# Performance work log

Measured on AMD Instinct MI355X. Metric: run time of the kernel, lower is better.

The kernel has to match this reference:

```python
import jax, jax.numpy as jnp
import numpy as np

B, S, H = 4, 2048, 1024
E, I, K = 8, 2048, 2


def setup_inputs() -> dict:
    key = jax.random.key(0)
    ks = jax.random.split(key, 6)
    return {
        "hidden_states": jax.random.normal(ks[0], (B, S, H), dtype=jnp.float32),
        "Wg": jax.random.normal(ks[1], (H, E), dtype=jnp.float32) * 0.02,
        "W1": jax.random.normal(ks[2], (E, H, I), dtype=jnp.float32) * 0.02,
        "b1": jnp.zeros((E, I), dtype=jnp.float32),
        "W2": jax.random.normal(ks[3], (E, I, H), dtype=jnp.float32) * 0.02,
        "b2": jnp.zeros((E, H), dtype=jnp.float32),
    }


def reference(hidden_states, Wg, W1, b1, W2, b2):
    b, s, h = hidden_states.shape
    x = hidden_states.reshape(-1, h)                      # [T, H]
    gate_logits = x @ Wg                                  # [T, E]
    gate_probs = jax.nn.softmax(gate_logits, axis=-1)
    topk_probs, topk_idx = jax.lax.top_k(gate_probs, K)   # [T, K]
    topk_probs = topk_probs / jnp.sum(topk_probs, axis=-1, keepdims=True)
    # dense combine weights [T, E] (zero where expert not selected)
    T = x.shape[0]
    w = jnp.zeros((T, E), dtype=x.dtype)
    w = w.at[jnp.arange(T)[:, None], topk_idx].set(topk_probs)
    # run every expert on all tokens (dense grouped-GEMM form), exact erf GELU
    h1 = jax.nn.gelu(jnp.einsum('th,ehi->eti', x, W1) + b1[:, None, :], approximate=False)  # [E, T, I]
    y = jnp.einsum('eti,eih->eth', h1, W2) + b2[:, None, :]                                  # [E, T, H]
    out = jnp.einsum('te,eth->th', w, y)                                                     # [T, H]
    return out.reshape(b, s, h)
```

## Files before the change

### kernel.cpp

```cpp
#include <hip/hip_runtime.h>
#include <math.h>

#define TOKS 8192
#define HD 1024
#define ID 2048
#define NE 8

typedef __bf16 bf16_t;
typedef __bf16 bf16x8 __attribute__((ext_vector_type(8)));
typedef float f32x4 __attribute__((ext_vector_type(4)));

#define GLOAD(gp, lp)                                                \
  __builtin_amdgcn_global_load_lds(                                  \
      (const __attribute__((address_space(1))) void*)(gp),           \
      (__attribute__((address_space(3))) void*)(lp), 16, 0, 0)

#define WAITV(N) asm volatile("s_waitcnt vmcnt(" #N ")" ::: "memory")
#define WAITL0() asm volatile("s_waitcnt lgkmcnt(0)" ::: "memory")

#define WS_COUNTS 0
#define WS_OFFSETS 32
#define WS_BTOK 128
#define WS_BW (128 + 65536)
#define WS_TE (128 + 2 * 65536)
#define WS_TW (128 + 3 * 65536)
#define WS_WL 263168ull
#define WS_BLKC 266240ull
#define WS_BLKB 270336ull
#define WS_POS 274432ull
#define WS_XB 524288ull
#define WS_H1 (WS_XB + 16777216ull)
#define WS_WT (WS_H1 + 67108864ull)
#define WS_Y (WS_WT + 33554432ull)

#define MAXWL 144
#define BM 128

__global__ __launch_bounds__(256) void gate_kernel(const float* __restrict__ x,
                                                   const float* __restrict__ Wg,
                                                   bf16_t* __restrict__ xb,
                                                   int* __restrict__ tok_e,
                                                   float* __restrict__ tok_w) {
  __shared__ float WgT[NE][HD];
  const int tid = threadIdx.x;
#pragma unroll
  for (int i = 0; i < NE * HD / 256; ++i) {
    const int idx = i * 256 + tid;
    WgT[idx & 7][idx >> 3] = Wg[idx];
  }
  __syncthreads();
  const int wv = tid >> 6;
  const int lane = tid & 63;
#pragma unroll
  for (int s = 0; s < 2; ++s) {
    const int t = blockIdx.x * 8 + wv * 2 + s;
    const float* xrow = x + (size_t)t * HD;
    bf16_t* xbrow = xb + (size_t)t * HD;
    float acc[NE];
#pragma unroll
    for (int e = 0; e < NE; ++e) acc[e] = 0.f;
#pragma unroll
    for (int i = 0; i < 16; ++i) {
      const int h = i * 64 + lane;
      const float xv = xrow[h];
      xbrow[h] = (bf16_t)xv;
#pragma unroll
      for (int e = 0; e < NE; ++e) acc[e] += xv * WgT[e][h];
    }
#pragma unroll
    for (int off = 32; off >= 1; off >>= 1) {
#pragma unroll
      for (int e = 0; e < NE; ++e) acc[e] += __shfl_xor(acc[e], off);
    }
    if (lane == 0) {
      int i1 = 0;
      float l1 = acc[0];
#pragma unroll
      for (int e = 1; e < NE; ++e)
        if (acc[e] > l1) { l1 = acc[e]; i1 = e; }
      int i2 = -1;
      float l2 = -3.4e38f;
#pragma unroll
      for (int e = 0; e < NE; ++e)
        if (e != i1 && acc[e] > l2) { l2 = acc[e]; i2 = e; }
      const float q = expf(l2 - l1);
      const float w1 = 1.f / (1.f + q);
      tok_e[2 * t] = i1;
      tok_e[2 * t + 1] = i2;
      tok_w[2 * t] = w1;
      tok_w[2 * t + 1] = q * w1;
    }
  }
}

__global__ __launch_bounds__(256) void hist_kernel(const int* __restrict__ tok_e,
                                                   int* __restrict__ blk_cnt) {
  __shared__ int wcnt[4][NE];
  const int tid = threadIdx.x;
  const int idx = blockIdx.x * 256 + tid;
  const int e = tok_e[idx];
  const int w = tid >> 6;
  const int lane = tid & 63;
#pragma unroll
  for (int e0 = 0; e0 < NE; ++e0) {
    const unsigned long long m = __ballot(e == e0);
    if (lane == 0) wcnt[w][e0] = __popcll(m);
  }
  __syncthreads();
  if (tid < NE)
    blk_cnt[blockIdx.x * NE + tid] =
        wcnt[0][tid] + wcnt[1][tid] + wcnt[2][tid] + wcnt[3][tid];
}

__global__ void scan_kernel(const int* __restrict__ blk_cnt, int* __restrict__ counts,
                            int* __restrict__ offsets, int* __restrict__ blk_base,
                            int* __restrict__ wl_e, int* __restrict__ wl_m,
                            int* __restrict__ n_work) {
  const int b = threadIdx.x;
  int c[NE], pre[NE], tot[NE];
#pragma unroll
  for (int e = 0; e < NE; ++e) c[e] = blk_cnt[b * NE + e];
#pragma unroll
  for (int e = 0; e < NE; ++e) {
    int v = c[e];
#pragma unroll
    for (int off = 1; off < 64; off <<= 1) {
      const int u = __shfl_up(v, off);
      if (b >= off) v += u;
    }
    pre[e] = v - c[e];
    tot[e] = __shfl(v, 63);
  }
  int off_[NE];
  int s = 0;
#pragma unroll
  for (int e = 0; e < NE; ++e) {
    off_[e] = s;
    s += tot[e];
  }
#pragma unroll
  for (int e = 0; e < NE; ++e) blk_base[b * NE + e] = off_[e] + pre[e];
  if (b == 0) {
    int idx = 0;
    for (int e = 0; e < NE; ++e) {
      counts[e] = tot[e];
      offsets[e] = off_[e];
      for (int m = 0; m < tot[e] && idx < MAXWL; m += BM) {
        wl_e[idx] = e;
        wl_m[idx] = m;
        ++idx;
      }
    }
    *n_work = idx;
  }
}

__global__ __launch_bounds__(256) void scatter_kernel(const int* __restrict__ tok_e,
                                                      const float* __restrict__ tok_w,
                                                      const int* __restrict__ blk_base,
                                                      int* __restrict__ bucket_tok,
                                                      float* __restrict__ bucket_w,
                                                      int* __restrict__ pos_of) {
  __shared__ int wcnt[4][NE];
  const int tid = threadIdx.x;
  const int idx = blockIdx.x * 256 + tid;
  const int e = tok_e[idx];
  const int w = tid >> 6;
  const int lane = tid & 63;
  unsigned long long mym = 0;
#pragma unroll
  for (int e0 = 0; e0 < NE; ++e0) {
    const unsigned long long m = __ballot(e == e0);
    if (lane == 0) wcnt[w][e0] = __popcll(m);
    if (e0 == e) mym = m;
  }
  __syncthreads();
  int base = blk_base[blockIdx.x * NE + e];
  for (int w2 = 0; w2 < w; ++w2) base += wcnt[w2][e];
  const int rank = __popcll(mym & ((1ull << lane) - 1ull));
  const int pos = base + rank;
  bucket_tok[pos] = idx >> 1;
  bucket_w[pos] = tok_w[idx];
  pos_of[idx] = pos;
}

__global__ __launch_bounds__(256) void transpose_convert_kernel(const float* __restrict__ src,
                                                                bf16_t* __restrict__ dst, int K,
                                                                int N) {
  __shared__ float tile[64][65];
  const int e = blockIdx.z;
  const int k0 = blockIdx.x * 64;
  const int n0 = blockIdx.y * 64;
  const float* s = src + (size_t)e * K * N;
  bf16_t* d = dst + (size_t)e * K * N;
  const int t = threadIdx.x;
  const int c = t & 63;
  const int r4 = t >> 6;
#pragma unroll
  for (int p = 0; p < 16; ++p) {
    const int r = p * 4 + r4;
    tile[r][c] = s[(size_t)(k0 + r) * N + n0 + c];
  }
  __syncthreads();
  const int kc = t & 7;
  const int nb = t >> 3;
#pragma unroll
  for (int p = 0; p < 2; ++p) {
    const int n = p * 32 + nb;
    bf16_t o[8];
#pragma unroll
    for (int j = 0; j < 8; ++j) o[j] = (bf16_t)tile[kc * 8 + j][n];
    *(uint4*)(d + (size_t)(n0 + n) * K + k0 + kc * 8) = *(uint4*)o;
  }
}


__global__ __launch_bounds__(256, 3) void gemm1_kernel(
    const bf16_t* __restrict__ xb, const bf16_t* __restrict__ W1T, const float* __restrict__ b1,
    const int* __restrict__ counts, const int* __restrict__ offsets,
    const int* __restrict__ bucket_tok, const int* __restrict__ wl_e,
    const int* __restrict__ wl_m, const int* __restrict__ n_work, bf16_t* __restrict__ h1) {
  const int widx = blockIdx.x;
  if (widx >= *n_work) return;
  const int e = wl_e[widx];
  const int m_base = wl_m[widx];
  const int n_e = counts[e];
  const int n_base = blockIdx.y * 128;
  const int off = offsets[e];

  __shared__ bf16_t As[3][128 * 32];
  __shared__ bf16_t Bs[3][128 * 32];

  const int tid = threadIdx.x;
  const int w = tid >> 6;
  const int lane = tid & 63;
  const int quad = lane >> 4;
  const int lrow = lane & 15;
  const int wm = w >> 1;
  const int wn = w & 1;

  const int srow = lane >> 2;
  const int kch = (((lane & 3) ^ ((lane >> 4) & 3)) * 8);
  int r0 = m_base + w * 32 + srow;
  int r1 = r0 + 16;
  if (r0 >= n_e) r0 = n_e - 1;
  if (r1 >= n_e) r1 = n_e - 1;
  const bf16_t* ga0 = xb + (size_t)bucket_tok[off + r0] * HD + kch;
  const bf16_t* ga1 = xb + (size_t)bucket_tok[off + r1] * HD + kch;
  const bf16_t* gb0 = W1T + ((size_t)e * ID + n_base + w * 32 + srow) * HD + kch;
  const bf16_t* gb1 = gb0 + (size_t)16 * HD;
  const int laofs0 = w * 1024 + lane * 8;
  const int laofs1 = laofs0 + 512;

  f32x4 acc[4][4];
#pragma unroll
  for (int mt = 0; mt < 4; ++mt)
#pragma unroll
    for (int nt = 0; nt < 4; ++nt)
#pragma unroll
      for (int r = 0; r < 4; ++r) acc[mt][nt][r] = 0.f;

#pragma unroll
  for (int p = 0; p < 2; ++p) {
    const size_t ko = (size_t)p * 32;
    GLOAD(ga0 + ko, &As[p][laofs0]);
    GLOAD(ga1 + ko, &As[p][laofs1]);
    GLOAD(gb0 + ko, &Bs[p][laofs0]);
    GLOAD(gb1 + ko, &Bs[p][laofs1]);
  }

  const int slot = (quad ^ ((lrow >> 2) & 3)) * 8;
  int cur = 0;
  int pre = 2;
#define NT1 (HD / 32)
  for (int kt = 0; kt < NT1; ++kt) {
    WAITL0();
    __builtin_amdgcn_s_barrier();
    if (kt + 2 < NT1) {
      const size_t ko = (size_t)(kt + 2) * 32;
      GLOAD(ga0 + ko, &As[pre][laofs0]);
      GLOAD(ga1 + ko, &As[pre][laofs1]);
      GLOAD(gb0 + ko, &Bs[pre][laofs0]);
      GLOAD(gb1 + ko, &Bs[pre][laofs1]);
      WAITV(8);
    } else if (kt + 1 < NT1) {
      WAITV(4);
    } else {
      WAITV(0);
    }
    __builtin_amdgcn_s_barrier();
    __builtin_amdgcn_sched_barrier(0);
    bf16x8 af[4], bfr[4];
#pragma unroll
    for (int i = 0; i < 4; ++i) {
      af[i] = *(const bf16x8*)(&As[cur][(wm * 64 + i * 16 + lrow) * 32 + slot]);
      bfr[i] = *(const bf16x8*)(&Bs[cur][(wn * 64 + i * 16 + lrow) * 32 + slot]);
    }
#pragma unroll
    for (int mt = 0; mt < 4; ++mt)
#pragma unroll
      for (int nt = 0; nt < 4; ++nt)
        acc[mt][nt] =
            __builtin_amdgcn_mfma_f32_16x16x32_bf16(af[mt], bfr[nt], acc[mt][nt], 0, 0, 0);
    cur = (cur == 2) ? 0 : cur + 1;
    pre = (pre == 2) ? 0 : pre + 1;
  }

#pragma unroll
  for (int mt = 0; mt < 4; ++mt) {
#pragma unroll
    for (int r = 0; r < 4; ++r) {
      const int gm = m_base + wm * 64 + mt * 16 + quad * 4 + r;
      if (gm < n_e) {
        bf16_t* orow = h1 + (size_t)(off + gm) * ID;
#pragma unroll
        for (int nt = 0; nt < 4; ++nt) {
          const int gi = n_base + wn * 64 + nt * 16 + lrow;
          float v = acc[mt][nt][r] + b1[e * ID + gi];
          v = 0.5f * v * (1.f + erff(v * 0.70710678118654752f));
          orow[gi] = (bf16_t)v;
        }
      }
    }
  }
}

__global__ __launch_bounds__(256, 3) void gemm2_kernel(
    const bf16_t* __restrict__ h1, const bf16_t* __restrict__ W2T, const float* __restrict__ b2,
    const int* __restrict__ counts, const int* __restrict__ offsets,
    const int* __restrict__ wl_e, const int* __restrict__ wl_m, const int* __restrict__ n_work,
    bf16_t* __restrict__ y) {
  const int widx = blockIdx.x;
  if (widx >= *n_work) return;
  const int e = wl_e[widx];
  const int m_base = wl_m[widx];
  const int n_e = counts[e];
  const int n_base = blockIdx.y * 128;
  const int off = offsets[e];

  __shared__ bf16_t As[3][128 * 32];
  __shared__ bf16_t Bs[3][128 * 32];

  const int tid = threadIdx.x;
  const int w = tid >> 6;
  const int lane = tid & 63;
  const int quad = lane >> 4;
  const int lrow = lane & 15;
  const int wm = w >> 1;
  const int wn = w & 1;

  const int srow = lane >> 2;
  const int kch = (((lane & 3) ^ ((lane >> 4) & 3)) * 8);
  int r0 = m_base + w * 32 + srow;
  int r1 = r0 + 16;
  if (r0 >= n_e) r0 = n_e - 1;
  if (r1 >= n_e) r1 = n_e - 1;
  const bf16_t* ga0 = h1 + (size_t)(off + r0) * ID + kch;
  const bf16_t* ga1 = h1 + (size_t)(off + r1) * ID + kch;
  const bf16_t* gb0 = W2T + ((size_t)e * HD + n_base + w * 32 + srow) * ID + kch;
  const bf16_t* gb1 = gb0 + (size_t)16 * ID;
  const int laofs0 = w * 1024 + lane * 8;
  const int laofs1 = laofs0 + 512;

  f32x4 acc[4][4];
#pragma unroll
  for (int mt = 0; mt < 4; ++mt)
#pragma unroll
    for (int nt = 0; nt < 4; ++nt)
#pragma unroll
      for (int r = 0; r < 4; ++r) acc[mt][nt][r] = 0.f;

#pragma unroll
  for (int p = 0; p < 2; ++p) {
    const size_t ko = (size_t)p * 32;
    GLOAD(ga0 + ko, &As[p][laofs0]);
    GLOAD(ga1 + ko, &As[p][laofs1]);
    GLOAD(gb0 + ko, &Bs[p][laofs0]);
    GLOAD(gb1 + ko, &Bs[p][laofs1]);
  }

  const int slot = (quad ^ ((lrow >> 2) & 3)) * 8;
  int cur = 0;
  int pre = 2;
#define NT2 (ID / 32)
  for (int kt = 0; kt < NT2; ++kt) {
    WAITL0();
    __builtin_amdgcn_s_barrier();
    if (kt + 2 < NT2) {
      const size_t ko = (size_t)(kt + 2) * 32;
      GLOAD(ga0 + ko, &As[pre][laofs0]);
      GLOAD(ga1 + ko, &As[pre][laofs1]);
      GLOAD(gb0 + ko, &Bs[pre][laofs0]);
      GLOAD(gb1 + ko, &Bs[pre][laofs1]);
      WAITV(8);
    } else if (kt + 1 < NT2) {
      WAITV(4);
    } else {
      WAITV(0);
    }
    __builtin_amdgcn_s_barrier();
    __builtin_amdgcn_sched_barrier(0);
    bf16x8 af[4], bfr[4];
#pragma unroll
    for (int i = 0; i < 4; ++i) {
      af[i] = *(const bf16x8*)(&As[cur][(wm * 64 + i * 16 + lrow) * 32 + slot]);
      bfr[i] = *(const bf16x8*)(&Bs[cur][(wn * 64 + i * 16 + lrow) * 32 + slot]);
    }
#pragma unroll
    for (int mt = 0; mt < 4; ++mt)
#pragma unroll
      for (int nt = 0; nt < 4; ++nt)
        acc[mt][nt] =
            __builtin_amdgcn_mfma_f32_16x16x32_bf16(af[mt], bfr[nt], acc[mt][nt], 0, 0, 0);
    cur = (cur == 2) ? 0 : cur + 1;
    pre = (pre == 2) ? 0 : pre + 1;
  }

#pragma unroll
  for (int mt = 0; mt < 4; ++mt) {
#pragma unroll
    for (int r = 0; r < 4; ++r) {
      const int gm = m_base + wm * 64 + mt * 16 + quad * 4 + r;
      if (gm < n_e) {
        bf16_t* orow = y + (size_t)(off + gm) * HD;
#pragma unroll
        for (int nt = 0; nt < 4; ++nt) {
          const int gh = n_base + wn * 64 + nt * 16 + lrow;
          orow[gh] = (bf16_t)(acc[mt][nt][r] + b2[e * HD + gh]);
        }
      }
    }
  }
}

__global__ __launch_bounds__(256) void combine_kernel(const bf16_t* __restrict__ y,
                                                      const int* __restrict__ pos_of,
                                                      const float* __restrict__ tok_w,
                                                      float* __restrict__ out) {
  const int gid = blockIdx.x * 256 + threadIdx.x;
  const int t = gid >> 7;
  const int c8 = (gid & 127) * 8;
  const int p1 = pos_of[2 * t];
  const int p2 = pos_of[2 * t + 1];
  const float w1 = tok_w[2 * t];
  const float w2 = tok_w[2 * t + 1];
  const bf16x8 a = *(const bf16x8*)(y + (size_t)p1 * HD + c8);
  const bf16x8 b = *(const bf16x8*)(y + (size_t)p2 * HD + c8);
  float* op = out + (size_t)t * HD + c8;
#pragma unroll
  for (int j = 0; j < 8; ++j) op[j] = w1 * (float)a[j] + w2 * (float)b[j];
}

extern "C" void kernel_launch(void* const* d_in, const int* in_sizes, int n_in,
                              void* d_out, int out_size, void* d_ws, size_t ws_size,
                              hipStream_t stream) {
  const float* x = (const float*)d_in[0];
  const float* Wg = (const float*)d_in[1];
  const float* W1 = (const float*)d_in[2];
  const float* b1 = (const float*)d_in[3];
  const float* W2 = (const float*)d_in[4];
  const float* b2 = (const float*)d_in[5];
  float* out = (float*)d_out;
  char* ws = (char*)d_ws;

  int* counts = (int*)(ws + WS_COUNTS);
  int* offsets = (int*)(ws + WS_OFFSETS);
  int* bucket_tok = (int*)(ws + WS_BTOK);
  float* bucket_w = (float*)(ws + WS_BW);
  int* tok_e = (int*)(ws + WS_TE);
  float* tok_w = (float*)(ws + WS_TW);
  int* wl_e = (int*)(ws + WS_WL);
  int* wl_m = wl_e + MAXWL;
  int* n_work = wl_m + MAXWL;
  int* blk_cnt = (int*)(ws + WS_BLKC);
  int* blk_base = (int*)(ws + WS_BLKB);
  int* pos_of = (int*)(ws + WS_POS);
  bf16_t* xb = (bf16_t*)(ws + WS_XB);
  bf16_t* h1 = (bf16_t*)(ws + WS_H1);
  bf16_t* WT = (bf16_t*)(ws + WS_WT);
  bf16_t* y = (bf16_t*)(ws + WS_Y);

  gate_kernel<<<TOKS / 8, 256, 0, stream>>>(x, Wg, xb, tok_e, tok_w);
  hist_kernel<<<TOKS * 2 / 256, 256, 0, stream>>>(tok_e, blk_cnt);
  scan_kernel<<<1, 64, 0, stream>>>(blk_cnt, counts, offsets, blk_base, wl_e, wl_m, n_work);
  scatter_kernel<<<TOKS * 2 / 256, 256, 0, stream>>>(tok_e, tok_w, blk_base, bucket_tok,
                                                     bucket_w, pos_of);
  transpose_convert_kernel<<<dim3(HD / 64, ID / 64, NE), 256, 0, stream>>>(W1, WT, HD, ID);
  gemm1_kernel<<<dim3(MAXWL, ID / 128), 256, 0, stream>>>(xb, WT, b1, counts, offsets, bucket_tok,
                                                          wl_e, wl_m, n_work, h1);
  transpose_convert_kernel<<<dim3(ID / 64, HD / 64, NE), 256, 0, stream>>>(W2, WT, ID, HD);
  gemm2_kernel<<<dim3(MAXWL, HD / 128), 256, 0, stream>>>(h1, WT, b2, counts, offsets, wl_e,
                                                          wl_m, n_work, y);
  combine_kernel<<<TOKS * HD / (256 * 8), 256, 0, stream>>>(y, pos_of, tok_w, out);
}
```

Before: 469.2 us.

## Vectorize epilogue stores via swapped MFMA operands, fast erf, float4 loads

Both grouped GEMMs swap the MFMA A/B operands so each lane's accumulator holds four consecutive output columns of one row. That lets the epilogue issue 8-byte packed bf16 stores and float4 bias loads in place of scattered 2-byte stores. GEMM1's GELU replaces erff with an Abramowitz-Stegun polynomial plus __expf, trading some accuracy (around 1e-7 absolute erf error) for fewer instructions. The weight transpose kernel now reads with float4 loads, and the combine kernel writes with float4 stores.

```diff
diff --git a/kernel.cpp b/kernel.cpp
--- a/kernel.cpp
+++ b/kernel.cpp
@@ -17,6 +17,19 @@
 
 #define WAITV(N) asm volatile("s_waitcnt vmcnt(" #N ")" ::: "memory")
 #define WAITL0() asm volatile("s_waitcnt lgkmcnt(0)" ::: "memory")
+
+__device__ __forceinline__ float gelu_exact(float v) {
+  const float u = v * 0.70710678118654752f;
+  const float a = fabsf(u);
+  const float t = 1.f / (1.f + 0.3275911f * a);
+  const float poly =
+      t * (0.254829592f +
+           t * (-0.284496736f +
+                t * (1.421413741f + t * (-1.453152027f + t * 1.061405429f))));
+  float er = 1.f - poly * __expf(-a * a);
+  er = copysignf(er, u);
+  return 0.5f * v * (1.f + er);
+}
 
 #define WS_COUNTS 0
 #define WS_OFFSETS 32
@@ -194,12 +207,16 @@
   const float* s = src + (size_t)e * K * N;
   bf16_t* d = dst + (size_t)e * K * N;
   const int t = threadIdx.x;
-  const int c = t & 63;
-  const int r4 = t >> 6;
-#pragma unroll
-  for (int p = 0; p < 16; ++p) {
-    const int r = p * 4 + r4;
-    tile[r][c] = s[(size_t)(k0 + r) * N + n0 + c];
+  const int c4 = (t & 15) * 4;
+  const int rr = t >> 4;
+#pragma unroll
+  for (int p = 0; p < 4; ++p) {
+    const int r = p * 16 + rr;
+    const float4 v = *(const float4*)(s + (size_t)(k0 + r) * N + n0 + c4);
+    tile[r][c4] = v.x;
+    tile[r][c4 + 1] = v.y;
+    tile[r][c4 + 2] = v.z;
+    tile[r][c4 + 3] = v.w;
   }
   __syncthreads();
   const int kc = t & 7;
@@ -301,25 +318,25 @@
 #pragma unroll
       for (int nt = 0; nt < 4; ++nt)
         acc[mt][nt] =
-            __builtin_amdgcn_mfma_f32_16x16x32_bf16(af[mt], bfr[nt], acc[mt][nt], 0, 0, 0);
+            __builtin_amdgcn_mfma_f32_16x16x32_bf16(bfr[nt], af[mt], acc[mt][nt], 0, 0, 0);
     cur = (cur == 2) ? 0 : cur + 1;
     pre = (pre == 2) ? 0 : pre + 1;
   }
 
 #pragma unroll
   for (int mt = 0; mt < 4; ++mt) {
-#pragma unroll
-    for (int r = 0; r < 4; ++r) {
-      const int gm = m_base + wm * 64 + mt * 16 + quad * 4 + r;
-      if (gm < n_e) {
-        bf16_t* orow = h1 + (size_t)(off + gm) * ID;
-#pragma unroll
-        for (int nt = 0; nt < 4; ++nt) {
-          const int gi = n_base + wn * 64 + nt * 16 + lrow;
-          float v = acc[mt][nt][r] + b1[e * ID + gi];
-          v = 0.5f * v * (1.f + erff(v * 0.70710678118654752f));
-          orow[gi] = (bf16_t)v;
-        }
+    const int gm = m_base + wm * 64 + mt * 16 + lrow;
+    if (gm < n_e) {
+      bf16_t* orow = h1 + (size_t)(off + gm) * ID;
+#pragma unroll
+      for (int nt = 0; nt < 4; ++nt) {
+        const int gi0 = n_base + wn * 64 + nt * 16 + quad * 4;
+        const float4 bb = *(const float4*)(b1 + e * ID + gi0);
+        const float bv[4] = {bb.x, bb.y, bb.z, bb.w};
+        bf16_t o[4];
+#pragma unroll
+        for (int r = 0; r < 4; ++r) o[r] = (bf16_t)gelu_exact(acc[mt][nt][r] + bv[r]);
+        *(uint2*)(orow + gi0) = *(uint2*)o;
       }
     }
   }
@@ -411,23 +428,25 @@
 #pragma unroll
       for (int nt = 0; nt < 4; ++nt)
         acc[mt][nt] =
-            __builtin_amdgcn_mfma_f32_16x16x32_bf16(af[mt], bfr[nt], acc[mt][nt], 0, 0, 0);
+            __builtin_amdgcn_mfma_f32_16x16x32_bf16(bfr[nt], af[mt], acc[mt][nt], 0, 0, 0);
     cur = (cur == 2) ? 0 : cur + 1;
     pre = (pre == 2) ? 0 : pre + 1;
   }
 
 #pragma unroll
   for (int mt = 0; mt < 4; ++mt) {
-#pragma unroll
-    for (int r = 0; r < 4; ++r) {
-      const int gm = m_base + wm * 64 + mt * 16 + quad * 4 + r;
-      if (gm < n_e) {
-        bf16_t* orow = y + (size_t)(off + gm) * HD;
-#pragma unroll
-        for (int nt = 0; nt < 4; ++nt) {
-          const int gh = n_base + wn * 64 + nt * 16 + lrow;
-          orow[gh] = (bf16_t)(acc[mt][nt][r] + b2[e * HD + gh]);
-        }
+    const int gm = m_base + wm * 64 + mt * 16 + lrow;
+    if (gm < n_e) {
+      bf16_t* orow = y + (size_t)(off + gm) * HD;
+#pragma unroll
+      for (int nt = 0; nt < 4; ++nt) {
+        const int gi0 = n_base + wn * 64 + nt * 16 + quad * 4;
+        const float4 bb = *(const float4*)(b2 + e * HD + gi0);
+        const float bv[4] = {bb.x, bb.y, bb.z, bb.w};
+        bf16_t o[4];
+#pragma unroll
+        for (int r = 0; r < 4; ++r) o[r] = (bf16_t)(acc[mt][nt][r] + bv[r]);
+        *(uint2*)(orow + gi0) = *(uint2*)o;
       }
     }
   }
@@ -447,8 +466,11 @@
   const bf16x8 a = *(const bf16x8*)(y + (size_t)p1 * HD + c8);
   const bf16x8 b = *(const bf16x8*)(y + (size_t)p2 * HD + c8);
   float* op = out + (size_t)t * HD + c8;
-#pragma unroll
-  for (int j = 0; j < 8; ++j) op[j] = w1 * (float)a[j] + w2 * (float)b[j];
+  float ov[8];
+#pragma unroll
+  for (int j = 0; j < 8; ++j) ov[j] = w1 * (float)a[j] + w2 * (float)b[j];
+  *(float4*)op = make_float4(ov[0], ov[1], ov[2], ov[3]);
+  *(float4*)(op + 4) = make_float4(ov[4], ov[5], ov[6], ov[7]);
 }
 
 extern "C" void kernel_launch(void* const* d_in, const int* in_sizes, int n_in,
```

Result: faster. 447.8 us (-4.6%).
